# Performance work log

Hardware: AMD Instinct MI355X
Metric: run time of the kernel (lower is better)

## Reference

```python
import jax, jax.numpy as jnp
import numpy as np

NUM_USERS = 100000
NUM_JOBS = 50000
NUM_EDGES = 2000000
NUM_LABELS = 500000
HID = 128
USER_DIM = 512
JOB_DIM = 768
BN_EPS = 1e-5


def setup_inputs() -> dict:
    key = jax.random.key(0)
    ks = iter(jax.random.split(key, 40))
    d = {}
    d['user_x'] = jax.random.normal(next(ks), (NUM_USERS, USER_DIM), jnp.float32)
    d['job_x'] = jax.random.normal(next(ks), (NUM_JOBS, JOB_DIM), jnp.float32)
    d['user_W'] = jax.random.normal(next(ks), (HID, USER_DIM), jnp.float32) * 0.05
    d['user_b'] = jax.random.normal(next(ks), (HID,), jnp.float32)
    d['user_gamma'] = jax.random.uniform(next(ks), (HID,), jnp.float32)
    d['user_beta'] = jax.random.normal(next(ks), (HID,), jnp.float32)
    d['user_mean'] = jax.random.normal(next(ks), (HID,), jnp.float32)
    d['user_var'] = jax.random.uniform(next(ks), (HID,), jnp.float32)
    d['job_W'] = jax.random.normal(next(ks), (HID, JOB_DIM), jnp.float32) * 0.05
    d['job_b'] = jax.random.normal(next(ks), (HID,), jnp.float32)
    d['job_gamma'] = jax.random.uniform(next(ks), (HID,), jnp.float32)
    d['job_beta'] = jax.random.normal(next(ks), (HID,), jnp.float32)
    d['job_mean'] = jax.random.normal(next(ks), (HID,), jnp.float32)
    d['job_var'] = jax.random.uniform(next(ks), (HID,), jnp.float32)
    for nm in ['l1_rates_Wl', 'l1_rates_Wr', 'l1_rev_Wl', 'l1_rev_Wr',
               'l2_rates_Wl', 'l2_rates_Wr', 'l2_rev_Wl', 'l2_rev_Wr']:
        d[nm] = jax.random.normal(next(ks), (HID, HID), jnp.float32) * 0.08
    for nm in ['l1_rates_bl', 'l1_rev_bl', 'l2_rates_bl', 'l2_rev_bl']:
        d[nm] = jax.random.normal(next(ks), (HID,), jnp.float32) * 0.05
    d['rates_src'] = jax.random.randint(next(ks), (NUM_EDGES,), 0, NUM_USERS, jnp.int64 if jax.config.jax_enable_x64 else jnp.int32)
    d['rates_dst'] = jax.random.randint(next(ks), (NUM_EDGES,), 0, NUM_JOBS, jnp.int32)
    d['label_src'] = jax.random.randint(next(ks), (NUM_LABELS,), 0, NUM_USERS, jnp.int32)
    d['label_dst'] = jax.random.randint(next(ks), (NUM_LABELS,), 0, NUM_JOBS, jnp.int32)
    return d


def _mean_aggr(x_src, src_idx, dst_idx, num_dst):
    # scatter-mean of gathered source features onto destination nodes
    s = jax.ops.segment_sum(x_src[src_idx], dst_idx, num_segments=num_dst)
    cnt = jax.ops.segment_sum(jnp.ones(src_idx.shape[0], x_src.dtype), dst_idx, num_segments=num_dst)
    return s / jnp.maximum(cnt, 1.0)[:, None]


def _sage(x_src, x_dst, src_idx, dst_idx, Wl, bl, Wr):
    agg = _mean_aggr(x_src, src_idx, dst_idx, x_dst.shape[0])
    return agg @ Wl.T + bl + x_dst @ Wr.T


def _bn(x, gamma, beta, mean, var):
    return (x - mean) * (gamma * jax.lax.rsqrt(var + BN_EPS)) + beta


def reference(user_x, job_x, user_W, user_b, user_gamma, user_beta, user_mean, user_var,
              job_W, job_b, job_gamma, job_beta, job_mean, job_var,
              l1_rates_Wl, l1_rates_bl, l1_rates_Wr, l1_rev_Wl, l1_rev_bl, l1_rev_Wr,
              l2_rates_Wl, l2_rates_bl, l2_rates_Wr, l2_rev_Wl, l2_rev_bl, l2_rev_Wr,
              rates_src, rates_dst, label_src, label_dst):
    # node-type encoders: Linear -> BN(eval) -> ReLU  (dropout is identity in eval)
    u = jax.nn.relu(_bn(user_x @ user_W.T + user_b, user_gamma, user_beta, user_mean, user_var))
    j = jax.nn.relu(_bn(job_x @ job_W.T + job_b, job_gamma, job_beta, job_mean, job_var))
    # hetero SAGE layer 1: rates (user->job), rev_rates (job->user)
    j1 = jax.nn.relu(_sage(u, j, rates_src, rates_dst, l1_rates_Wl, l1_rates_bl, l1_rates_Wr))
    u1 = jax.nn.relu(_sage(j, u, rates_dst, rates_src, l1_rev_Wl, l1_rev_bl, l1_rev_Wr))
    # hetero SAGE layer 2 (no activation after, matches GNN.forward)
    j2 = _sage(u1, j1, rates_src, rates_dst, l2_rates_Wl, l2_rates_bl, l2_rates_Wr)
    u2 = _sage(j1, u1, rates_dst, rates_src, l2_rev_Wl, l2_rev_bl, l2_rev_Wr)
    # dot-product link classifier over label edges
    return jnp.sum(u2[label_src] * j2[label_dst], axis=1)
```

## Files before the change

kernel.cpp:

```cpp
#include <hip/hip_runtime.h>
#include <cstdint>
#include <cstddef>

#define HID 128
#define N_USERS 100000
#define N_JOBS  50000
#define N_EDGES 2000000
#define N_LABELS 500000

#define RBITS 8
#define RSIZE 256
#define NBJ ((N_JOBS  + RSIZE - 1) / RSIZE)
#define NBU ((N_USERS + RSIZE - 1) / RSIZE)
#define P1CHUNK 8192

#define TBU ((N_USERS + 63) / 64)
#define TBJ ((N_JOBS  + 63) / 64)
#define ABJ ((N_JOBS  + 3) / 4)
#define ABU ((N_USERS + 3) / 4)

typedef __attribute__((ext_vector_type(8))) short short8;
typedef __attribute__((ext_vector_type(4))) float f32x4;

__device__ __forceinline__ unsigned short f2b(float f) {
    union { float f; unsigned u; } v; v.f = f;
    unsigned r = v.u + 0x7FFFu + ((v.u >> 16) & 1u);
    return (unsigned short)(r >> 16);
}
__device__ __forceinline__ float b2f(unsigned h) {
    union { unsigned u; float f; } v; v.u = h << 16;
    return v.f;
}
__device__ __forceinline__ unsigned pk2(float lo, float hi) {
    return (unsigned)f2b(lo) | ((unsigned)f2b(hi) << 16);
}
__device__ __forceinline__ void gl_lds16(const void* g, void* l) {
    __builtin_amdgcn_global_load_lds(
        (const __attribute__((address_space(1))) unsigned int*)g,
        (__attribute__((address_space(3))) unsigned int*)l, 16, 0, 0);
}

__global__ __launch_bounds__(256) void cvt_weights(
    const float* __restrict__ uW, const float* __restrict__ jW,
    const float* __restrict__ a, const float* __restrict__ b,
    const float* __restrict__ c, const float* __restrict__ d,
    const float* __restrict__ e, const float* __restrict__ f,
    const float* __restrict__ g, const float* __restrict__ h,
    unsigned short* __restrict__ ow) {
    int i4 = blockIdx.x * 256 + threadIdx.x;
    if (i4 >= 73728) return;
    int i = i4 * 4;
    const float* src; int base;
    if (i < 65536)       { src = uW; base = 0; }
    else if (i < 163840) { src = jW; base = 65536; }
    else {
        int k = (i - 163840) >> 14;
        const float* s4 = (k < 4) ? ((k < 2) ? (k == 0 ? a : b) : (k == 2 ? c : d))
                                  : ((k < 6) ? (k == 4 ? e : f) : (k == 6 ? g : h));
        src = s4; base = 163840 + (k << 14);
    }
    float4 v = *reinterpret_cast<const float4*>(src + (i - base));
    *reinterpret_cast<uint2*>(ow + i) = make_uint2(pk2(v.x, v.y), pk2(v.z, v.w));
}

__global__ __launch_bounds__(256) void bucket_hist(const int* __restrict__ src,
                                                   const int* __restrict__ dst,
                                                   int nE, int* __restrict__ bcnt_j,
                                                   int* __restrict__ bcnt_u) {
    __shared__ int hj[NBJ];
    __shared__ int hu[NBU];
    int t = threadIdx.x;
    for (int i = t; i < NBJ; i += 256) hj[i] = 0;
    for (int i = t; i < NBU; i += 256) hu[i] = 0;
    __syncthreads();
    int i = blockIdx.x * blockDim.x + t;
    int stride = gridDim.x * blockDim.x;
    for (; i < nE; i += stride) {
        atomicAdd(&hj[dst[i] >> RBITS], 1);
        atomicAdd(&hu[src[i] >> RBITS], 1);
    }
    __syncthreads();
    for (int i2 = t; i2 < NBJ; i2 += 256) if (hj[i2]) atomicAdd(&bcnt_j[i2], hj[i2]);
    for (int i2 = t; i2 < NBU; i2 += 256) if (hu[i2]) atomicAdd(&bcnt_u[i2], hu[i2]);
}

__global__ __launch_bounds__(1024) void bucket_scan(int* __restrict__ bcnt_j, int* __restrict__ boff_j,
                                                    int* __restrict__ bcur_j,
                                                    int* __restrict__ bcnt_u, int* __restrict__ boff_u,
                                                    int* __restrict__ bcur_u) {
    int* bcnt = blockIdx.x ? bcnt_u : bcnt_j;
    int* boff = blockIdx.x ? boff_u : boff_j;
    int* bcur = blockIdx.x ? bcur_u : bcur_j;
    int n = blockIdx.x ? NBU : NBJ;
    __shared__ int sm[1024];
    int t = threadIdx.x;
    int v = (t < n) ? bcnt[t] : 0;
    sm[t] = v;
    __syncthreads();
    for (int d = 1; d < 1024; d <<= 1) {
        int q = (t >= d) ? sm[t - d] : 0;
        __syncthreads();
        sm[t] += q;
        __syncthreads();
    }
    if (t < n) { int e = sm[t] - v; boff[t] = e; bcur[t] = e; }
    if (t == 0) boff[n] = N_EDGES;
}

__global__ __launch_bounds__(256) void csr_pass1(const int* __restrict__ src,
                                                 const int* __restrict__ dst,
                                                 int nE, int* __restrict__ gcur_j,
                                                 int* __restrict__ gcur_u,
                                                 unsigned* __restrict__ stage_j,
                                                 unsigned* __restrict__ stage_u) {
    __shared__ int cur_j[NBJ];
    __shared__ int cur_u[NBU];
    int t = threadIdx.x;
    int e0 = blockIdx.x * P1CHUNK;
    int e1 = min(e0 + P1CHUNK, nE);
    for (int i = t; i < NBJ; i += 256) cur_j[i] = 0;
    for (int i = t; i < NBU; i += 256) cur_u[i] = 0;
    __syncthreads();
    for (int e = e0 + t; e < e1; e += 256) {
        atomicAdd(&cur_j[dst[e] >> RBITS], 1);
        atomicAdd(&cur_u[src[e] >> RBITS], 1);
    }
    __syncthreads();
    for (int i = t; i < NBJ; i += 256) {
        int c = cur_j[i];
        cur_j[i] = c ? atomicAdd(&gcur_j[i], c) : 0;
    }
    for (int i = t; i < NBU; i += 256) {
        int c = cur_u[i];
        cur_u[i] = c ? atomicAdd(&gcur_u[i], c) : 0;
    }
    __syncthreads();
    for (int e = e0 + t; e < e1; e += 256) {
        int d = dst[e], s = src[e];
        int pj = atomicAdd(&cur_j[d >> RBITS], 1);
        stage_j[pj] = ((unsigned)(d & (RSIZE - 1)) << 24) | (unsigned)s;
        int pu = atomicAdd(&cur_u[s >> RBITS], 1);
        stage_u[pu] = ((unsigned)(s & (RSIZE - 1)) << 24) | (unsigned)d;
    }
}

__global__ __launch_bounds__(256) void csr_pass2(
    const unsigned* __restrict__ stage_j, const int* __restrict__ boff_j,
    int* __restrict__ off_j, int* __restrict__ vals_j,
    const unsigned* __restrict__ stage_u, const int* __restrict__ boff_u,
    int* __restrict__ off_u, int* __restrict__ vals_u) {
    __shared__ int cnt[RSIZE];
    __shared__ int sc[RSIZE];
    __shared__ int cur[RSIZE];
    int borig = blockIdx.x, t = threadIdx.x;
    const unsigned* words; const int* boff; int* off; int* vals; int b; int nNodes;
    if (borig < NBJ) { words = stage_j; boff = boff_j; off = off_j; vals = vals_j; b = borig; nNodes = N_JOBS; }
    else             { words = stage_u; boff = boff_u; off = off_u; vals = vals_u; b = borig - NBJ; nNodes = N_USERS; }
    int node0 = b << RBITS;
    int sbeg = boff[b], send = boff[b + 1];
    cnt[t] = 0;
    __syncthreads();
    for (int e = sbeg + t; e < send; e += 256) {
        atomicAdd(&cnt[words[e] >> 24], 1);
    }
    __syncthreads();
    int v = cnt[t];
    sc[t] = v;
    __syncthreads();
    #pragma unroll
    for (int d = 1; d < RSIZE; d <<= 1) {
        int q = (t >= d) ? sc[t - d] : 0;
        __syncthreads();
        sc[t] += q;
        __syncthreads();
    }
    int node = node0 + t;
    if (node < nNodes) {
        int base = sbeg + sc[t] - v;
        off[node] = base;
        cur[t] = base;
    }
    __syncthreads();
    for (int e = sbeg + t; e < send; e += 256) {
        unsigned w = words[e];
        int slot = atomicAdd(&cur[w >> 24], 1);
        vals[slot] = (int)(w & 0xFFFFFFu);
    }
    if (t == 0 && borig == 0)   off_j[N_JOBS]  = N_EDGES;
    if (t == 0 && borig == NBJ) off_u[N_USERS] = N_EDGES;
}

__global__ __launch_bounds__(256) void aggregate2(
    const unsigned short* __restrict__ xJ, const int* __restrict__ offJ,
    const int* __restrict__ valsJ, unsigned short* __restrict__ outJ,
    const unsigned short* __restrict__ xU, const int* __restrict__ offU,
    const int* __restrict__ valsU, unsigned short* __restrict__ outU) {
    int bb = blockIdx.x;
    const unsigned short* x; const int* off; const int* vals; unsigned short* out;
    int nDst, node0;
    if (bb < ABJ) { x = xJ; off = offJ; vals = valsJ; out = outJ; nDst = N_JOBS;  node0 = bb * 4; }
    else          { x = xU; off = offU; vals = valsU; out = outU; nDst = N_USERS; node0 = (bb - ABJ) * 4; }
    int node = node0 + (threadIdx.x >> 6);
    if (node >= nDst) return;
    int lane = threadIdx.x & 63;
    int hl = lane & 31;
    int eo = lane >> 5;
    int beg = off[node], end = off[node + 1];
    float a0 = 0.f, a1 = 0.f, a2 = 0.f, a3 = 0.f;
    int e = beg;
    for (; e + 3 < end; e += 4) {
        int s0 = vals[e + eo], s1 = vals[e + 2 + eo];
        uint2 v0 = *reinterpret_cast<const uint2*>(x + (size_t)s0 * HID + hl * 4);
        uint2 v1 = *reinterpret_cast<const uint2*>(x + (size_t)s1 * HID + hl * 4);
        a0 += b2f(v0.x & 0xffffu) + b2f(v1.x & 0xffffu);
        a1 += b2f(v0.x >> 16)     + b2f(v1.x >> 16);
        a2 += b2f(v0.y & 0xffffu) + b2f(v1.y & 0xffffu);
        a3 += b2f(v0.y >> 16)     + b2f(v1.y >> 16);
    }
    for (; e < end; e += 2) {
        int ee = e + eo;
        if (ee < end) {
            int s = vals[ee];
            uint2 v = *reinterpret_cast<const uint2*>(x + (size_t)s * HID + hl * 4);
            a0 += b2f(v.x & 0xffffu);
            a1 += b2f(v.x >> 16);
            a2 += b2f(v.y & 0xffffu);
            a3 += b2f(v.y >> 16);
        }
    }
    a0 += __shfl_xor(a0, 32, 64);
    a1 += __shfl_xor(a1, 32, 64);
    a2 += __shfl_xor(a2, 32, 64);
    a3 += __shfl_xor(a3, 32, 64);
    if (eo == 0) {
        float inv = 1.0f / fmaxf((float)(end - beg), 1.0f);
        *reinterpret_cast<uint2*>(out + (size_t)node * HID + hl * 4) =
            make_uint2(pk2(a0 * inv, a1 * inv), pk2(a2 * inv, a3 * inv));
    }
}

__global__ __launch_bounds__(256) void encoder_mfma(
    const float* __restrict__ Xu, const unsigned short* __restrict__ Wbu,
    const float* __restrict__ bu, const float* __restrict__ gu,
    const float* __restrict__ beu, const float* __restrict__ mu,
    const float* __restrict__ vu,
    const float* __restrict__ Xj, const unsigned short* __restrict__ Wbj,
    const float* __restrict__ bj, const float* __restrict__ gj,
    const float* __restrict__ bej, const float* __restrict__ mj,
    const float* __restrict__ vj,
    unsigned short* __restrict__ outU, unsigned short* __restrict__ outJ) {
    __shared__ float lds[2][4096];
    const float *X, *bias, *gamma, *beta, *mean, *var;
    const unsigned short* Wb; unsigned short* out;
    int M, K, m0;
    if (blockIdx.x < TBU) {
        X = Xu; Wb = Wbu; bias = bu; gamma = gu; beta = beu; mean = mu; var = vu;
        out = outU; M = N_USERS; K = 512; m0 = blockIdx.x * 64;
    } else {
        X = Xj; Wb = Wbj; bias = bj; gamma = gj; beta = bej; mean = mj; var = vj;
        out = outJ; M = N_JOBS; K = 768; m0 = (blockIdx.x - TBU) * 64;
    }
    int tid = threadIdx.x;
    int w = tid >> 6, lane = tid & 63;
    int lrow = lane & 15, lgrp = lane >> 4;
    f32x4 acc[4][2];
    #pragma unroll
    for (int m = 0; m < 4; ++m)
        #pragma unroll
        for (int n = 0; n < 2; ++n) acc[m][n] = (f32x4){0.f, 0.f, 0.f, 0.f};

    const unsigned short* wp[2];
    #pragma unroll
    for (int n = 0; n < 2; ++n)
        wp[n] = Wb + (size_t)(w * 32 + n * 16 + lrow) * K + lgrp * 8;

    auto STAGE = [&](int t, int b) {
        int k0 = t << 6;
        #pragma unroll
        for (int c = 0; c < 4; ++c) {
            int unit = c * 256 + tid;
            int row = unit >> 4, u = unit & 15;
            int gr = m0 + row; if (gr > M - 1) gr = M - 1;
            const float* g = X + (size_t)gr * K + k0 + ((u ^ (row & 15)) << 2);
            gl_lds16(g, (void*)&lds[b][unit * 4]);
        }
    };
    auto LOADW = [&](int t, short8* dst) {
        int k0 = t << 6;
        #pragma unroll
        for (int ks = 0; ks < 2; ++ks)
            #pragma unroll
            for (int n = 0; n < 2; ++n)
                dst[ks * 2 + n] = *reinterpret_cast<const short8*>(wp[n] + k0 + ks * 32);
    };

    int nt = K >> 6;
    short8 bfc[4], bfn[4];
    LOADW(0, bfc);
    STAGE(0, 0);
    __syncthreads();
    for (int t = 0; t < nt; ++t) {
        if (t + 1 < nt) { LOADW(t + 1, bfn); STAGE(t + 1, (t + 1) & 1); }
        const float* bufp = &lds[t & 1][0];
        #pragma unroll
        for (int ks = 0; ks < 2; ++ks) {
            int p = ks * 4 + lgrp;
            #pragma unroll
            for (int m = 0; m < 4; ++m) {
                int row = m * 16 + lrow;
                int swz = row & 15;
                float4 ra = *reinterpret_cast<const float4*>(bufp + row * 64 + (((2 * p)     ^ swz) << 2));
                float4 rb = *reinterpret_cast<const float4*>(bufp + row * 64 + (((2 * p + 1) ^ swz) << 2));
                union { unsigned u[4]; short8 s; } r;
                r.u[0] = pk2(ra.x, ra.y); r.u[1] = pk2(ra.z, ra.w);
                r.u[2] = pk2(rb.x, rb.y); r.u[3] = pk2(rb.z, rb.w);
                acc[m][0] = __builtin_amdgcn_mfma_f32_16x16x32_bf16(bfc[ks * 2 + 0], r.s, acc[m][0], 0, 0, 0);
                acc[m][1] = __builtin_amdgcn_mfma_f32_16x16x32_bf16(bfc[ks * 2 + 1], r.s, acc[m][1], 0, 0, 0);
            }
        }
        __syncthreads();
        if (t + 1 < nt) {
            #pragma unroll
            for (int i = 0; i < 4; ++i) bfc[i] = bfn[i];
        }
    }

    float sc[2][4], sh[2][4];
    #pragma unroll
    for (int n = 0; n < 2; ++n)
        #pragma unroll
        for (int j = 0; j < 4; ++j) {
            int gc = w * 32 + n * 16 + lgrp * 4 + j;
            float s = gamma[gc] * rsqrtf(var[gc] + 1e-5f);
            sc[n][j] = s;
            sh[n][j] = (bias[gc] - mean[gc]) * s + beta[gc];
        }
    #pragma unroll
    for (int m = 0; m < 4; ++m) {
        int row = m0 + m * 16 + lrow;
        if (row < M) {
            #pragma unroll
            for (int n = 0; n < 2; ++n) {
                float v0 = fmaxf(acc[m][n][0] * sc[n][0] + sh[n][0], 0.f);
                float v1 = fmaxf(acc[m][n][1] * sc[n][1] + sh[n][1], 0.f);
                float v2 = fmaxf(acc[m][n][2] * sc[n][2] + sh[n][2], 0.f);
                float v3 = fmaxf(acc[m][n][3] * sc[n][3] + sh[n][3], 0.f);
                *reinterpret_cast<uint2*>(out + (size_t)row * HID + w * 32 + n * 16 + lgrp * 4) =
                    make_uint2(pk2(v0, v1), pk2(v2, v3));
            }
        }
    }
}

__global__ __launch_bounds__(256) void sage_mfma(
    const unsigned short* __restrict__ AaggJ, const unsigned short* __restrict__ BxJ,
    const unsigned short* __restrict__ WAj, const unsigned short* __restrict__ WBj,
    const float* __restrict__ blJ, unsigned short* __restrict__ outJ,
    const unsigned short* __restrict__ AaggU, const unsigned short* __restrict__ BxU,
    const unsigned short* __restrict__ WAu, const unsigned short* __restrict__ WBu,
    const float* __restrict__ blU, unsigned short* __restrict__ outU,
    int doRelu) {
    __shared__ unsigned short lds[2][4096];
    const unsigned short *Aagg, *Bx, *WA, *WB; const float* bl; unsigned short* out;
    int M, m0;
    if (blockIdx.x < TBJ) {
        Aagg = AaggJ; Bx = BxJ; WA = WAj; WB = WBj; bl = blJ; out = outJ;
        M = N_JOBS; m0 = blockIdx.x * 64;
    } else {
        Aagg = AaggU; Bx = BxU; WA = WAu; WB = WBu; bl = blU; out = outU;
        M = N_USERS; m0 = (blockIdx.x - TBJ) * 64;
    }
    int tid = threadIdx.x;
    int w = tid >> 6, lane = tid & 63;
    int lrow = lane & 15, lgrp = lane >> 4;
    f32x4 acc[4][2];
    #pragma unroll
    for (int m = 0; m < 4; ++m)
        #pragma unroll
        for (int n = 0; n < 2; ++n) acc[m][n] = (f32x4){0.f, 0.f, 0.f, 0.f};

    auto STAGE = [&](int s, int b) {
        const unsigned short* Ap = (s < 2) ? Aagg : Bx;
        int k0 = (s & 1) << 6;
        #pragma unroll
        for (int c = 0; c < 2; ++c) {
            int unit = c * 256 + tid;
            int row = unit >> 3, u = unit & 7;
            int gr = m0 + row; if (gr > M - 1) gr = M - 1;
            const unsigned short* g = Ap + (size_t)gr * HID + k0 + ((u ^ (row & 7)) << 3);
            gl_lds16(g, (void*)&lds[b][unit * 8]);
        }
    };
    auto LOADW = [&](int s, short8* dst) {
        const unsigned short* Wp = (s < 2) ? WA : WB;
        int k0 = (s & 1) << 6;
        #pragma unroll
        for (int ks = 0; ks < 2; ++ks)
            #pragma unroll
            for (int n = 0; n < 2; ++n)
                dst[ks * 2 + n] = *reinterpret_cast<const short8*>(
                    Wp + (size_t)(w * 32 + n * 16 + lrow) * HID + k0 + ks * 32 + lgrp * 8);
    };

    short8 bfc[4], bfn[4];
    LOADW(0, bfc);
    STAGE(0, 0);
    __syncthreads();
    #pragma unroll
    for (int s = 0; s < 4; ++s) {
        if (s < 3) { LOADW(s + 1, bfn); STAGE(s + 1, (s + 1) & 1); }
        const unsigned short* bufp = &lds[s & 1][0];
        #pragma unroll
        for (int ks = 0; ks < 2; ++ks) {
            int p = ks * 4 + lgrp;
            #pragma unroll
            for (int m = 0; m < 4; ++m) {
                int row = m * 16 + lrow;
                short8 af = *reinterpret_cast<const short8*>(bufp + row * 64 + ((p ^ (row & 7)) << 3));
                acc[m][0] = __builtin_amdgcn_mfma_f32_16x16x32_bf16(bfc[ks * 2 + 0], af, acc[m][0], 0, 0, 0);
                acc[m][1] = __builtin_amdgcn_mfma_f32_16x16x32_bf16(bfc[ks * 2 + 1], af, acc[m][1], 0, 0, 0);
            }
        }
        __syncthreads();
        if (s < 3) {
            #pragma unroll
            for (int i = 0; i < 4; ++i) bfc[i] = bfn[i];
        }
    }

    float blv[2][4];
    #pragma unroll
    for (int n = 0; n < 2; ++n)
        #pragma unroll
        for (int j = 0; j < 4; ++j)
            blv[n][j] = bl[w * 32 + n * 16 + lgrp * 4 + j];
    #pragma unroll
    for (int m = 0; m < 4; ++m) {
        int row = m0 + m * 16 + lrow;
        if (row < M) {
            #pragma unroll
            for (int n = 0; n < 2; ++n) {
                float v[4];
                #pragma unroll
                for (int j = 0; j < 4; ++j) {
                    float x = acc[m][n][j] + blv[n][j];
                    v[j] = doRelu ? fmaxf(x, 0.f) : x;
                }
                *reinterpret_cast<uint2*>(out + (size_t)row * HID + w * 32 + n * 16 + lgrp * 4) =
                    make_uint2(pk2(v[0], v[1]), pk2(v[2], v[3]));
            }
        }
    }
}

__global__ __launch_bounds__(256) void dot_kernel(const unsigned short* __restrict__ U,
                                                  const unsigned short* __restrict__ J,
                                                  const int* __restrict__ ls,
                                                  const int* __restrict__ ld,
                                                  float* __restrict__ out, int nL) {
    int ew = (int)((blockIdx.x * blockDim.x + threadIdx.x) >> 5);
    int hl = threadIdx.x & 31;
    if (ew >= nL) return;
    int a = ls[ew], c = ld[ew];
    uint2 uv = *reinterpret_cast<const uint2*>(U + (size_t)a * HID + hl * 4);
    uint2 jv = *reinterpret_cast<const uint2*>(J + (size_t)c * HID + hl * 4);
    float p = b2f(uv.x & 0xffffu) * b2f(jv.x & 0xffffu)
            + b2f(uv.x >> 16)     * b2f(jv.x >> 16)
            + b2f(uv.y & 0xffffu) * b2f(jv.y & 0xffffu)
            + b2f(uv.y >> 16)     * b2f(jv.y >> 16);
    #pragma unroll
    for (int s = 16; s > 0; s >>= 1) p += __shfl_xor(p, s, 64);
    if (hl == 0) out[ew] = p;
}

extern "C" void kernel_launch(void* const* d_in, const int* in_sizes, int n_in,
                              void* d_out, int out_size, void* d_ws, size_t ws_size,
                              hipStream_t stream) {
    const float* user_x     = (const float*)d_in[0];
    const float* job_x      = (const float*)d_in[1];
    const float* user_W     = (const float*)d_in[2];
    const float* user_b     = (const float*)d_in[3];
    const float* user_gamma = (const float*)d_in[4];
    const float* user_beta  = (const float*)d_in[5];
    const float* user_mean  = (const float*)d_in[6];
    const float* user_var   = (const float*)d_in[7];
    const float* job_W      = (const float*)d_in[8];
    const float* job_b      = (const float*)d_in[9];
    const float* job_gamma  = (const float*)d_in[10];
    const float* job_beta   = (const float*)d_in[11];
    const float* job_mean   = (const float*)d_in[12];
    const float* job_var    = (const float*)d_in[13];
    const float* l1_rates_Wl = (const float*)d_in[14];
    const float* l1_rates_Wr = (const float*)d_in[15];
    const float* l1_rev_Wl   = (const float*)d_in[16];
    const float* l1_rev_Wr   = (const float*)d_in[17];
    const float* l2_rates_Wl = (const float*)d_in[18];
    const float* l2_rates_Wr = (const float*)d_in[19];
    const float* l2_rev_Wl   = (const float*)d_in[20];
    const float* l2_rev_Wr   = (const float*)d_in[21];
    const float* l1_rates_bl = (const float*)d_in[22];
    const float* l1_rev_bl   = (const float*)d_in[23];
    const float* l2_rates_bl = (const float*)d_in[24];
    const float* l2_rev_bl   = (const float*)d_in[25];
    const int* rates_src = (const int*)d_in[26];
    const int* rates_dst = (const int*)d_in[27];
    const int* label_src = (const int*)d_in[28];
    const int* label_dst = (const int*)d_in[29];

    char* ws = (char*)d_ws;
    size_t o = 0;
    auto alloc = [&](size_t bytes) -> void* {
        void* p = ws + o;
        o = (o + bytes + 511) & ~(size_t)511;
        return p;
    };
    unsigned short* u_bf = (unsigned short*)alloc((size_t)N_USERS * HID * 2);
    unsigned short* j_bf = (unsigned short*)alloc((size_t)N_JOBS  * HID * 2);
    unsigned short* u1   = (unsigned short*)alloc((size_t)N_USERS * HID * 2);
    unsigned short* j1   = (unsigned short*)alloc((size_t)N_JOBS  * HID * 2);
    unsigned short* aggU = (unsigned short*)alloc((size_t)N_USERS * HID * 2);
    unsigned short* aggJ = (unsigned short*)alloc((size_t)N_JOBS  * HID * 2);
    unsigned short* u2b  = (unsigned short*)alloc((size_t)N_USERS * HID * 2);
    unsigned short* j2b  = (unsigned short*)alloc((size_t)N_JOBS  * HID * 2);
    int* vals_j = (int*)alloc((size_t)N_EDGES * 4);
    int* vals_u = (int*)alloc((size_t)N_EDGES * 4);
    unsigned* stage_j = (unsigned*)alloc((size_t)N_EDGES * 4);
    unsigned* stage_u = (unsigned*)alloc((size_t)N_EDGES * 4);
    int* off_j  = (int*)alloc((size_t)(N_JOBS + 1) * 4);
    int* off_u  = (int*)alloc((size_t)(N_USERS + 1) * 4);
    int* bcnt_j = (int*)alloc((size_t)(NBJ + 1) * 4);
    int* bcnt_u = (int*)alloc((size_t)(NBU + 1) * 4);
    int* boff_j = (int*)alloc((size_t)(NBJ + 1) * 4);
    int* boff_u = (int*)alloc((size_t)(NBU + 1) * 4);
    int* bcur_j = (int*)alloc((size_t)(NBJ + 1) * 4);
    int* bcur_u = (int*)alloc((size_t)(NBU + 1) * 4);
    unsigned short* wbf = (unsigned short*)alloc((size_t)294912 * 2);
    (void)ws_size; (void)n_in; (void)in_sizes; (void)out_size;

    const unsigned short* uWb = wbf;
    const unsigned short* jWb = wbf + 65536;
    const unsigned short* w8  = wbf + 163840;

    cvt_weights<<<288, 256, 0, stream>>>(user_W, job_W,
        l1_rates_Wl, l1_rates_Wr, l1_rev_Wl, l1_rev_Wr,
        l2_rates_Wl, l2_rates_Wr, l2_rev_Wl, l2_rev_Wr, wbf);

    hipMemsetAsync(bcnt_j, 0, (size_t)(NBJ + 1) * 4, stream);
    hipMemsetAsync(bcnt_u, 0, (size_t)(NBU + 1) * 4, stream);
    bucket_hist<<<512, 256, 0, stream>>>(rates_src, rates_dst, N_EDGES, bcnt_j, bcnt_u);
    bucket_scan<<<2, 1024, 0, stream>>>(bcnt_j, boff_j, bcur_j, bcnt_u, boff_u, bcur_u);
    csr_pass1<<<(N_EDGES + P1CHUNK - 1) / P1CHUNK, 256, 0, stream>>>(
        rates_src, rates_dst, N_EDGES, bcur_j, bcur_u, stage_j, stage_u);
    csr_pass2<<<NBJ + NBU, 256, 0, stream>>>(stage_j, boff_j, off_j, vals_j,
                                             stage_u, boff_u, off_u, vals_u);

    encoder_mfma<<<TBU + TBJ, 256, 0, stream>>>(
        user_x, uWb, user_b, user_gamma, user_beta, user_mean, user_var,
        job_x, jWb, job_b, job_gamma, job_beta, job_mean, job_var,
        u_bf, j_bf);

    aggregate2<<<ABJ + ABU, 256, 0, stream>>>(u_bf, off_j, vals_j, aggJ,
                                              j_bf, off_u, vals_u, aggU);
    sage_mfma<<<TBJ + TBU, 256, 0, stream>>>(
        aggJ, j_bf, w8 + 0 * 16384, w8 + 1 * 16384, l1_rates_bl, j1,
        aggU, u_bf, w8 + 2 * 16384, w8 + 3 * 16384, l1_rev_bl,   u1, 1);

    aggregate2<<<ABJ + ABU, 256, 0, stream>>>(u1, off_j, vals_j, aggJ,
                                              j1, off_u, vals_u, aggU);
    sage_mfma<<<TBJ + TBU, 256, 0, stream>>>(
        aggJ, j1, w8 + 4 * 16384, w8 + 5 * 16384, l2_rates_bl, j2b,
        aggU, u1, w8 + 6 * 16384, w8 + 7 * 16384, l2_rev_bl,   u2b, 0);

    dot_kernel<<<(N_LABELS * 32 + 255) / 256, 256, 0, stream>>>(
        u2b, j2b, label_src, label_dst, (float*)d_out, N_LABELS);
}
```

Before: 682.9 us.

## Fuse neighbor mean-aggregation into SAGE MFMA kernel and fold memsets into weight conversion

Each SAGE block now gathers and averages the neighbor features for its 64 destination rows straight into an LDS A-tile, then runs the MFMA GEMM against the aggregated and root features. This drops the separate aggregate kernel and the global round trip for the aggregated buffers in both layers. The bucket-count memsets are also moved into an extra block of the weight-conversion kernel, removing two launches. In exchange, the gather now runs with 64-row blocks, one wave per row in turn, which may cut memory-level parallelism compared with the dedicated aggregate kernel, and the GEMM cannot start until all gathers in the block finish.

```diff
diff --git a/kernel.cpp b/kernel.cpp
--- a/kernel.cpp
+++ b/kernel.cpp
@@ -16,8 +16,6 @@
 
 #define TBU ((N_USERS + 63) / 64)
 #define TBJ ((N_JOBS  + 63) / 64)
-#define ABJ ((N_JOBS  + 3) / 4)
-#define ABU ((N_USERS + 3) / 4)
 
 typedef __attribute__((ext_vector_type(8))) short short8;
 typedef __attribute__((ext_vector_type(4))) float f32x4;
@@ -46,7 +44,13 @@
     const float* __restrict__ c, const float* __restrict__ d,
     const float* __restrict__ e, const float* __restrict__ f,
     const float* __restrict__ g, const float* __restrict__ h,
-    unsigned short* __restrict__ ow) {
+    unsigned short* __restrict__ ow,
+    int* __restrict__ bcnt_j, int* __restrict__ bcnt_u) {
+    if (blockIdx.x == 288) {
+        for (int i = threadIdx.x; i <= NBJ; i += 256) bcnt_j[i] = 0;
+        for (int i = threadIdx.x; i <= NBU; i += 256) bcnt_u[i] = 0;
+        return;
+    }
     int i4 = blockIdx.x * 256 + threadIdx.x;
     if (i4 >= 73728) return;
     int i = i4 * 4;
@@ -188,55 +192,6 @@
     }
     if (t == 0 && borig == 0)   off_j[N_JOBS]  = N_EDGES;
     if (t == 0 && borig == NBJ) off_u[N_USERS] = N_EDGES;
-}
-
-__global__ __launch_bounds__(256) void aggregate2(
-    const unsigned short* __restrict__ xJ, const int* __restrict__ offJ,
-    const int* __restrict__ valsJ, unsigned short* __restrict__ outJ,
-    const unsigned short* __restrict__ xU, const int* __restrict__ offU,
-    const int* __restrict__ valsU, unsigned short* __restrict__ outU) {
-    int bb = blockIdx.x;
-    const unsigned short* x; const int* off; const int* vals; unsigned short* out;
-    int nDst, node0;
-    if (bb < ABJ) { x = xJ; off = offJ; vals = valsJ; out = outJ; nDst = N_JOBS;  node0 = bb * 4; }
-    else          { x = xU; off = offU; vals = valsU; out = outU; nDst = N_USERS; node0 = (bb - ABJ) * 4; }
-    int node = node0 + (threadIdx.x >> 6);
-    if (node >= nDst) return;
-    int lane = threadIdx.x & 63;
-    int hl = lane & 31;
-    int eo = lane >> 5;
-    int beg = off[node], end = off[node + 1];
-    float a0 = 0.f, a1 = 0.f, a2 = 0.f, a3 = 0.f;
-    int e = beg;
-    for (; e + 3 < end; e += 4) {
-        int s0 = vals[e + eo], s1 = vals[e + 2 + eo];
-        uint2 v0 = *reinterpret_cast<const uint2*>(x + (size_t)s0 * HID + hl * 4);
-        uint2 v1 = *reinterpret_cast<const uint2*>(x + (size_t)s1 * HID + hl * 4);
-        a0 += b2f(v0.x & 0xffffu) + b2f(v1.x & 0xffffu);
-        a1 += b2f(v0.x >> 16)     + b2f(v1.x >> 16);
-        a2 += b2f(v0.y & 0xffffu) + b2f(v1.y & 0xffffu);
-        a3 += b2f(v0.y >> 16)     + b2f(v1.y >> 16);
-    }
-    for (; e < end; e += 2) {
-        int ee = e + eo;
-        if (ee < end) {
-            int s = vals[ee];
-            uint2 v = *reinterpret_cast<const uint2*>(x + (size_t)s * HID + hl * 4);
-            a0 += b2f(v.x & 0xffffu);
-            a1 += b2f(v.x >> 16);
-            a2 += b2f(v.y & 0xffffu);
-            a3 += b2f(v.y >> 16);
-        }
-    }
-    a0 += __shfl_xor(a0, 32, 64);
-    a1 += __shfl_xor(a1, 32, 64);
-    a2 += __shfl_xor(a2, 32, 64);
-    a3 += __shfl_xor(a3, 32, 64);
-    if (eo == 0) {
-        float inv = 1.0f / fmaxf((float)(end - beg), 1.0f);
-        *reinterpret_cast<uint2*>(out + (size_t)node * HID + hl * 4) =
-            make_uint2(pk2(a0 * inv, a1 * inv), pk2(a2 * inv, a3 * inv));
-    }
 }
 
 __global__ __launch_bounds__(256) void encoder_mfma(
@@ -352,76 +307,136 @@
     }
 }
 
-__global__ __launch_bounds__(256) void sage_mfma(
-    const unsigned short* __restrict__ AaggJ, const unsigned short* __restrict__ BxJ,
+__global__ __launch_bounds__(256) void sage_fused(
+    const unsigned short* __restrict__ xJ, const int* __restrict__ offJ,
+    const int* __restrict__ valsJ, const unsigned short* __restrict__ BxJ,
     const unsigned short* __restrict__ WAj, const unsigned short* __restrict__ WBj,
     const float* __restrict__ blJ, unsigned short* __restrict__ outJ,
-    const unsigned short* __restrict__ AaggU, const unsigned short* __restrict__ BxU,
+    const unsigned short* __restrict__ xU, const int* __restrict__ offU,
+    const int* __restrict__ valsU, const unsigned short* __restrict__ BxU,
     const unsigned short* __restrict__ WAu, const unsigned short* __restrict__ WBu,
     const float* __restrict__ blU, unsigned short* __restrict__ outU,
     int doRelu) {
-    __shared__ unsigned short lds[2][4096];
-    const unsigned short *Aagg, *Bx, *WA, *WB; const float* bl; unsigned short* out;
-    int M, m0;
+    __shared__ unsigned short Atile[64 * 128];
+    __shared__ unsigned short Bst[2][64 * 64];
+    const unsigned short *x, *Bx, *WA, *WB; const int *off, *vals;
+    const float* bl; unsigned short* out; int M, m0;
     if (blockIdx.x < TBJ) {
-        Aagg = AaggJ; Bx = BxJ; WA = WAj; WB = WBj; bl = blJ; out = outJ;
-        M = N_JOBS; m0 = blockIdx.x * 64;
+        x = xJ; off = offJ; vals = valsJ; Bx = BxJ; WA = WAj; WB = WBj;
+        bl = blJ; out = outJ; M = N_JOBS; m0 = blockIdx.x * 64;
     } else {
-        Aagg = AaggU; Bx = BxU; WA = WAu; WB = WBu; bl = blU; out = outU;
-        M = N_USERS; m0 = (blockIdx.x - TBJ) * 64;
+        x = xU; off = offU; vals = valsU; Bx = BxU; WA = WAu; WB = WBu;
+        bl = blU; out = outU; M = N_USERS; m0 = (blockIdx.x - TBJ) * 64;
     }
     int tid = threadIdx.x;
     int w = tid >> 6, lane = tid & 63;
     int lrow = lane & 15, lgrp = lane >> 4;
+
+    #pragma unroll
+    for (int c = 0; c < 4; ++c) {
+        int q = c * 256 + tid;
+        int buf = q >> 9;
+        int unit = q & 511;
+        int row = unit >> 3, u = unit & 7;
+        int gr = m0 + row; if (gr > M - 1) gr = M - 1;
+        const unsigned short* g = Bx + (size_t)gr * HID + (buf << 6) + ((u ^ (row & 7)) << 3);
+        gl_lds16(g, (void*)(&Bst[buf][0] + unit * 8));
+    }
+
+    const unsigned short* wrow[2];
+    #pragma unroll
+    for (int n = 0; n < 2; ++n)
+        wrow[n] = (size_t)(w * 32 + n * 16 + lrow) * HID + lgrp * 8 + (const unsigned short*)nullptr + 0;
+    size_t woff[2];
+    #pragma unroll
+    for (int n = 0; n < 2; ++n)
+        woff[n] = (size_t)(w * 32 + n * 16 + lrow) * HID + lgrp * 8;
+    short8 bfc[4], bfn[4];
+    #pragma unroll
+    for (int ks = 0; ks < 2; ++ks)
+        #pragma unroll
+        for (int n = 0; n < 2; ++n)
+            bfc[ks * 2 + n] = *reinterpret_cast<const short8*>(WA + woff[n] + ks * 32);
+
+    int hl = lane & 31;
+    int eo = lane >> 5;
+    for (int i = 0; i < 16; ++i) {
+        int row = w * 16 + i;
+        int node = m0 + row;
+        if (node >= M) break;
+        int beg = off[node], end = off[node + 1];
+        float a0 = 0.f, a1 = 0.f, a2 = 0.f, a3 = 0.f;
+        int e = beg;
+        for (; e + 7 < end; e += 8) {
+            int s0 = vals[e + eo],     s1 = vals[e + 2 + eo];
+            int s2 = vals[e + 4 + eo], s3 = vals[e + 6 + eo];
+            uint2 v0 = *reinterpret_cast<const uint2*>(x + (size_t)s0 * HID + hl * 4);
+            uint2 v1 = *reinterpret_cast<const uint2*>(x + (size_t)s1 * HID + hl * 4);
+            uint2 v2 = *reinterpret_cast<const uint2*>(x + (size_t)s2 * HID + hl * 4);
+            uint2 v3 = *reinterpret_cast<const uint2*>(x + (size_t)s3 * HID + hl * 4);
+            a0 += b2f(v0.x & 0xffffu) + b2f(v1.x & 0xffffu) + b2f(v2.x & 0xffffu) + b2f(v3.x & 0xffffu);
+            a1 += b2f(v0.x >> 16)     + b2f(v1.x >> 16)     + b2f(v2.x >> 16)     + b2f(v3.x >> 16);
+            a2 += b2f(v0.y & 0xffffu) + b2f(v1.y & 0xffffu) + b2f(v2.y & 0xffffu) + b2f(v3.y & 0xffffu);
+            a3 += b2f(v0.y >> 16)     + b2f(v1.y >> 16)     + b2f(v2.y >> 16)     + b2f(v3.y >> 16);
+        }
+        for (; e < end; e += 2) {
+            int ee = e + eo;
+            if (ee < end) {
+                int s = vals[ee];
+                uint2 v = *reinterpret_cast<const uint2*>(x + (size_t)s * HID + hl * 4);
+                a0 += b2f(v.x & 0xffffu);
+                a1 += b2f(v.x >> 16);
+                a2 += b2f(v.y & 0xffffu);
+                a3 += b2f(v.y >> 16);
+            }
+        }
+        a0 += __shfl_xor(a0, 32, 64);
+        a1 += __shfl_xor(a1, 32, 64);
+        a2 += __shfl_xor(a2, 32, 64);
+        a3 += __shfl_xor(a3, 32, 64);
+        if (eo == 0) {
+            float inv = 1.0f / fmaxf((float)(end - beg), 1.0f);
+            int su = (hl >> 1) ^ i;
+            *reinterpret_cast<uint2*>(Atile + row * 128 + su * 8 + (hl & 1) * 4) =
+                make_uint2(pk2(a0 * inv, a1 * inv), pk2(a2 * inv, a3 * inv));
+        }
+    }
+    __syncthreads();
+
     f32x4 acc[4][2];
     #pragma unroll
     for (int m = 0; m < 4; ++m)
         #pragma unroll
         for (int n = 0; n < 2; ++n) acc[m][n] = (f32x4){0.f, 0.f, 0.f, 0.f};
 
-    auto STAGE = [&](int s, int b) {
-        const unsigned short* Ap = (s < 2) ? Aagg : Bx;
-        int k0 = (s & 1) << 6;
-        #pragma unroll
-        for (int c = 0; c < 2; ++c) {
-            int unit = c * 256 + tid;
-            int row = unit >> 3, u = unit & 7;
-            int gr = m0 + row; if (gr > M - 1) gr = M - 1;
-            const unsigned short* g = Ap + (size_t)gr * HID + k0 + ((u ^ (row & 7)) << 3);
-            gl_lds16(g, (void*)&lds[b][unit * 8]);
-        }
-    };
-    auto LOADW = [&](int s, short8* dst) {
-        const unsigned short* Wp = (s < 2) ? WA : WB;
-        int k0 = (s & 1) << 6;
-        #pragma unroll
-        for (int ks = 0; ks < 2; ++ks)
-            #pragma unroll
-            for (int n = 0; n < 2; ++n)
-                dst[ks * 2 + n] = *reinterpret_cast<const short8*>(
-                    Wp + (size_t)(w * 32 + n * 16 + lrow) * HID + k0 + ks * 32 + lgrp * 8);
-    };
-
-    short8 bfc[4], bfn[4];
-    LOADW(0, bfc);
-    STAGE(0, 0);
-    __syncthreads();
     #pragma unroll
     for (int s = 0; s < 4; ++s) {
-        if (s < 3) { LOADW(s + 1, bfn); STAGE(s + 1, (s + 1) & 1); }
-        const unsigned short* bufp = &lds[s & 1][0];
+        if (s < 3) {
+            const unsigned short* Wn = (s + 1 < 2) ? WA : WB;
+            int k0n = ((s + 1) & 1) << 6;
+            #pragma unroll
+            for (int ks = 0; ks < 2; ++ks)
+                #pragma unroll
+                for (int n = 0; n < 2; ++n)
+                    bfn[ks * 2 + n] = *reinterpret_cast<const short8*>(Wn + woff[n] + k0n + ks * 32);
+        }
         #pragma unroll
         for (int ks = 0; ks < 2; ++ks) {
             int p = ks * 4 + lgrp;
             #pragma unroll
             for (int m = 0; m < 4; ++m) {
                 int row = m * 16 + lrow;
-                short8 af = *reinterpret_cast<const short8*>(bufp + row * 64 + ((p ^ (row & 7)) << 3));
+                short8 af;
+                if (s < 2) {
+                    int gp = s * 8 + p;
+                    af = *reinterpret_cast<const short8*>(Atile + row * 128 + ((gp ^ (row & 15)) * 8));
+                } else {
+                    af = *reinterpret_cast<const short8*>(&Bst[s & 1][0] + row * 64 + ((p ^ (row & 7)) << 3));
+                }
                 acc[m][0] = __builtin_amdgcn_mfma_f32_16x16x32_bf16(bfc[ks * 2 + 0], af, acc[m][0], 0, 0, 0);
                 acc[m][1] = __builtin_amdgcn_mfma_f32_16x16x32_bf16(bfc[ks * 2 + 1], af, acc[m][1], 0, 0, 0);
             }
         }
-        __syncthreads();
         if (s < 3) {
             #pragma unroll
             for (int i = 0; i < 4; ++i) bfc[i] = bfn[i];
@@ -443,8 +458,8 @@
                 float v[4];
                 #pragma unroll
                 for (int j = 0; j < 4; ++j) {
-                    float x = acc[m][n][j] + blv[n][j];
-                    v[j] = doRelu ? fmaxf(x, 0.f) : x;
+                    float xv = acc[m][n][j] + blv[n][j];
+                    v[j] = doRelu ? fmaxf(xv, 0.f) : xv;
                 }
                 *reinterpret_cast<uint2*>(out + (size_t)row * HID + w * 32 + n * 16 + lgrp * 4) =
                     make_uint2(pk2(v[0], v[1]), pk2(v[2], v[3]));
@@ -518,8 +533,6 @@
     unsigned short* j_bf = (unsigned short*)alloc((size_t)N_JOBS  * HID * 2);
     unsigned short* u1   = (unsigned short*)alloc((size_t)N_USERS * HID * 2);
     unsigned short* j1   = (unsigned short*)alloc((size_t)N_JOBS  * HID * 2);
-    unsigned short* aggU = (unsigned short*)alloc((size_t)N_USERS * HID * 2);
-    unsigned short* aggJ = (unsigned short*)alloc((size_t)N_JOBS  * HID * 2);
     unsigned short* u2b  = (unsigned short*)alloc((size_t)N_USERS * HID * 2);
     unsigned short* j2b  = (unsigned short*)alloc((size_t)N_JOBS  * HID * 2);
     int* vals_j = (int*)alloc((size_t)N_EDGES * 4);
@@ -541,12 +554,10 @@
     const unsigned short* jWb = wbf + 65536;
     const unsigned short* w8  = wbf + 163840;
 
-    cvt_weights<<<288, 256, 0, stream>>>(user_W, job_W,
+    cvt_weights<<<289, 256, 0, stream>>>(user_W, job_W,
         l1_rates_Wl, l1_rates_Wr, l1_rev_Wl, l1_rev_Wr,
-        l2_rates_Wl, l2_rates_Wr, l2_rev_Wl, l2_rev_Wr, wbf);
-
-    hipMemsetAsync(bcnt_j, 0, (size_t)(NBJ + 1) * 4, stream);
-    hipMemsetAsync(bcnt_u, 0, (size_t)(NBU + 1) * 4, stream);
+        l2_rates_Wl, l2_rates_Wr, l2_rev_Wl, l2_rev_Wr, wbf, bcnt_j, bcnt_u);
+
     bucket_hist<<<512, 256, 0, stream>>>(rates_src, rates_dst, N_EDGES, bcnt_j, bcnt_u);
     bucket_scan<<<2, 1024, 0, stream>>>(bcnt_j, boff_j, bcur_j, bcnt_u, boff_u, bcur_u);
     csr_pass1<<<(N_EDGES + P1CHUNK - 1) / P1CHUNK, 256, 0, stream>>>(
@@ -559,17 +570,13 @@
         job_x, jWb, job_b, job_gamma, job_beta, job_mean, job_var,
         u_bf, j_bf);
 
-    aggregate2<<<ABJ + ABU, 256, 0, stream>>>(u_bf, off_j, vals_j, aggJ,
-                                              j_bf, off_u, vals_u, aggU);
-    sage_mfma<<<TBJ + TBU, 256, 0, stream>>>(
-        aggJ, j_bf, w8 + 0 * 16384, w8 + 1 * 16384, l1_rates_bl, j1,
-        aggU, u_bf, w8 + 2 * 16384, w8 + 3 * 16384, l1_rev_bl,   u1, 1);
-
-    aggregate2<<<ABJ + ABU, 256, 0, stream>>>(u1, off_j, vals_j, aggJ,
-                                              j1, off_u, vals_u, aggU);
-    sage_mfma<<<TBJ + TBU, 256, 0, stream>>>(
-        aggJ, j1, w8 + 4 * 16384, w8 + 5 * 16384, l2_rates_bl, j2b,
-        aggU, u1, w8 + 6 * 16384, w8 + 7 * 16384, l2_rev_bl,   u2b, 0);
+    sage_fused<<<TBJ + TBU, 256, 0, stream>>>(
+        u_bf, off_j, vals_j, j_bf, w8 + 0 * 16384, w8 + 1 * 16384, l1_rates_bl, j1,
+        j_bf, off_u, vals_u, u_bf, w8 + 2 * 16384, w8 + 3 * 16384, l1_rev_bl,   u1, 1);
+
+    sage_fused<<<TBJ + TBU, 256, 0, stream>>>(
+        u1, off_j, vals_j, j1, w8 + 4 * 16384, w8 + 5 * 16384, l2_rates_bl, j2b,
+        j1, off_u, vals_u, u1, w8 + 6 * 16384, w8 + 7 * 16384, l2_rev_bl,   u2b, 0);
 
     dot_kernel<<<(N_LABELS * 32 + 255) / 256, 256, 0, stream>>>(
         u2b, j2b, label_src, label_dst, (float*)d_out, N_LABELS);
```

Result: slower. 725.3 us (+6.2%).

## Split aggregation rows across two wavefronts and fold memsets into weight conversion

Applied to the files above, without the earlier changes.

The aggregate kernel now assigns two wavefronts per destination node, each covering half of the 128-wide feature row, with four edges in flight per wave instead of two. This raises memory-level parallelism for the gather-heavy mean aggregation, at the cost of an extra shuffle reduction step and twice as many blocks. Separately, the two hipMemsetAsync calls for the bucket counters are replaced by an extra block in the weight-conversion kernel, removing two small launches.

```diff
diff --git a/kernel.cpp b/kernel.cpp
--- a/kernel.cpp
+++ b/kernel.cpp
@@ -16,8 +16,8 @@
 
 #define TBU ((N_USERS + 63) / 64)
 #define TBJ ((N_JOBS  + 63) / 64)
-#define ABJ ((N_JOBS  + 3) / 4)
-#define ABU ((N_USERS + 3) / 4)
+#define AB2J ((N_JOBS  + 1) / 2)
+#define AB2U ((N_USERS + 1) / 2)
 
 typedef __attribute__((ext_vector_type(8))) short short8;
 typedef __attribute__((ext_vector_type(4))) float f32x4;
@@ -46,7 +46,13 @@
     const float* __restrict__ c, const float* __restrict__ d,
     const float* __restrict__ e, const float* __restrict__ f,
     const float* __restrict__ g, const float* __restrict__ h,
-    unsigned short* __restrict__ ow) {
+    unsigned short* __restrict__ ow,
+    int* __restrict__ bcnt_j, int* __restrict__ bcnt_u) {
+    if (blockIdx.x == 288) {
+        for (int i = threadIdx.x; i <= NBJ; i += 256) bcnt_j[i] = 0;
+        for (int i = threadIdx.x; i <= NBU; i += 256) bcnt_u[i] = 0;
+        return;
+    }
     int i4 = blockIdx.x * 256 + threadIdx.x;
     if (i4 >= 73728) return;
     int i = i4 * 4;
@@ -198,43 +204,46 @@
     int bb = blockIdx.x;
     const unsigned short* x; const int* off; const int* vals; unsigned short* out;
     int nDst, node0;
-    if (bb < ABJ) { x = xJ; off = offJ; vals = valsJ; out = outJ; nDst = N_JOBS;  node0 = bb * 4; }
-    else          { x = xU; off = offU; vals = valsU; out = outU; nDst = N_USERS; node0 = (bb - ABJ) * 4; }
-    int node = node0 + (threadIdx.x >> 6);
+    if (bb < AB2J) { x = xJ; off = offJ; vals = valsJ; out = outJ; nDst = N_JOBS;  node0 = bb * 2; }
+    else           { x = xU; off = offU; vals = valsU; out = outU; nDst = N_USERS; node0 = (bb - AB2J) * 2; }
+    int wid = threadIdx.x >> 6;
+    int node = node0 + (wid >> 1);
     if (node >= nDst) return;
+    int half = wid & 1;
     int lane = threadIdx.x & 63;
-    int hl = lane & 31;
-    int eo = lane >> 5;
+    int hl = lane & 15;
+    int eo = lane >> 4;
+    const unsigned short* xb = x + half * 64 + hl * 4;
     int beg = off[node], end = off[node + 1];
     float a0 = 0.f, a1 = 0.f, a2 = 0.f, a3 = 0.f;
     int e = beg;
-    for (; e + 3 < end; e += 4) {
-        int s0 = vals[e + eo], s1 = vals[e + 2 + eo];
-        uint2 v0 = *reinterpret_cast<const uint2*>(x + (size_t)s0 * HID + hl * 4);
-        uint2 v1 = *reinterpret_cast<const uint2*>(x + (size_t)s1 * HID + hl * 4);
+    for (; e + 7 < end; e += 8) {
+        int s0 = vals[e + eo], s1 = vals[e + 4 + eo];
+        uint2 v0 = *reinterpret_cast<const uint2*>(xb + (size_t)s0 * HID);
+        uint2 v1 = *reinterpret_cast<const uint2*>(xb + (size_t)s1 * HID);
         a0 += b2f(v0.x & 0xffffu) + b2f(v1.x & 0xffffu);
         a1 += b2f(v0.x >> 16)     + b2f(v1.x >> 16);
         a2 += b2f(v0.y & 0xffffu) + b2f(v1.y & 0xffffu);
         a3 += b2f(v0.y >> 16)     + b2f(v1.y >> 16);
     }
-    for (; e < end; e += 2) {
+    for (; e < end; e += 4) {
         int ee = e + eo;
         if (ee < end) {
             int s = vals[ee];
-            uint2 v = *reinterpret_cast<const uint2*>(x + (size_t)s * HID + hl * 4);
+            uint2 v = *reinterpret_cast<const uint2*>(xb + (size_t)s * HID);
             a0 += b2f(v.x & 0xffffu);
             a1 += b2f(v.x >> 16);
             a2 += b2f(v.y & 0xffffu);
             a3 += b2f(v.y >> 16);
         }
     }
-    a0 += __shfl_xor(a0, 32, 64);
-    a1 += __shfl_xor(a1, 32, 64);
-    a2 += __shfl_xor(a2, 32, 64);
-    a3 += __shfl_xor(a3, 32, 64);
+    a0 += __shfl_xor(a0, 16, 64); a0 += __shfl_xor(a0, 32, 64);
+    a1 += __shfl_xor(a1, 16, 64); a1 += __shfl_xor(a1, 32, 64);
+    a2 += __shfl_xor(a2, 16, 64); a2 += __shfl_xor(a2, 32, 64);
+    a3 += __shfl_xor(a3, 16, 64); a3 += __shfl_xor(a3, 32, 64);
     if (eo == 0) {
         float inv = 1.0f / fmaxf((float)(end - beg), 1.0f);
-        *reinterpret_cast<uint2*>(out + (size_t)node * HID + hl * 4) =
+        *reinterpret_cast<uint2*>(out + (size_t)node * HID + half * 64 + hl * 4) =
             make_uint2(pk2(a0 * inv, a1 * inv), pk2(a2 * inv, a3 * inv));
     }
 }
@@ -541,12 +550,10 @@
     const unsigned short* jWb = wbf + 65536;
     const unsigned short* w8  = wbf + 163840;
 
-    cvt_weights<<<288, 256, 0, stream>>>(user_W, job_W,
+    cvt_weights<<<289, 256, 0, stream>>>(user_W, job_W,
         l1_rates_Wl, l1_rates_Wr, l1_rev_Wl, l1_rev_Wr,
-        l2_rates_Wl, l2_rates_Wr, l2_rev_Wl, l2_rev_Wr, wbf);
-
-    hipMemsetAsync(bcnt_j, 0, (size_t)(NBJ + 1) * 4, stream);
-    hipMemsetAsync(bcnt_u, 0, (size_t)(NBU + 1) * 4, stream);
+        l2_rates_Wl, l2_rates_Wr, l2_rev_Wl, l2_rev_Wr, wbf, bcnt_j, bcnt_u);
+
     bucket_hist<<<512, 256, 0, stream>>>(rates_src, rates_dst, N_EDGES, bcnt_j, bcnt_u);
     bucket_scan<<<2, 1024, 0, stream>>>(bcnt_j, boff_j, bcur_j, bcnt_u, boff_u, bcur_u);
     csr_pass1<<<(N_EDGES + P1CHUNK - 1) / P1CHUNK, 256, 0, stream>>>(
@@ -559,14 +566,14 @@
         job_x, jWb, job_b, job_gamma, job_beta, job_mean, job_var,
         u_bf, j_bf);
 
-    aggregate2<<<ABJ + ABU, 256, 0, stream>>>(u_bf, off_j, vals_j, aggJ,
-                                              j_bf, off_u, vals_u, aggU);
+    aggregate2<<<AB2J + AB2U, 256, 0, stream>>>(u_bf, off_j, vals_j, aggJ,
+                                                j_bf, off_u, vals_u, aggU);
     sage_mfma<<<TBJ + TBU, 256, 0, stream>>>(
         aggJ, j_bf, w8 + 0 * 16384, w8 + 1 * 16384, l1_rates_bl, j1,
         aggU, u_bf, w8 + 2 * 16384, w8 + 3 * 16384, l1_rev_bl,   u1, 1);
 
-    aggregate2<<<ABJ + ABU, 256, 0, stream>>>(u1, off_j, vals_j, aggJ,
-                                              j1, off_u, vals_u, aggU);
+    aggregate2<<<AB2J + AB2U, 256, 0, stream>>>(u1, off_j, vals_j, aggJ,
+                                                j1, off_u, vals_u, aggU);
     sage_mfma<<<TBJ + TBU, 256, 0, stream>>>(
         aggJ, j1, w8 + 4 * 16384, w8 + 5 * 16384, l2_rates_bl, j2b,
         aggU, u1, w8 + 6 * 16384, w8 + 7 * 16384, l2_rev_bl,   u2b, 0);
```

After: 722.3 us. 1.06x slower.
